# Performance work log

Hardware: AMD Instinct MI355X
Metric: run time of the kernel (lower is better)

## Reference

```python
import jax, jax.numpy as jnp
import numpy as np

B, S, E, D, H, L = 128, 50, 512, 1024, 16, 4
V, NU, NF, NR = 100000, 50000, 10000, 5
DK = D // H
FF = 4 * D


def _pe(S, D):
    # FranchisePositionalEncoding: two interleaved sin/cos halves (chrono + release*1.5)
    half = D // 2
    pos = jnp.arange(S, dtype=jnp.float32)[:, None]
    div = jnp.exp(jnp.arange(0, half, 2, dtype=jnp.float32) * (-np.log(10000.0) / half))
    def il(a):
        return jnp.stack([jnp.sin(a), jnp.cos(a)], axis=-1).reshape(S, half)
    return jnp.concatenate([il(pos * div), il(pos * div * 1.5)], axis=-1)  # [S, D]


def _ln(x, g, b):
    m = x.mean(-1, keepdims=True)
    v = ((x - m) ** 2).mean(-1, keepdims=True)
    return (x - m) * jax.lax.rsqrt(v + 1e-5) * g + b


def _gelu(x):
    return jax.nn.gelu(x, approximate=False)


def setup_inputs() -> dict:
    key = jax.random.key(0)
    ks = iter(jax.random.split(key, 64))
    def p(shape, s=0.02):
        return jax.random.normal(next(ks), shape, jnp.float32) * s
    inp = {
        'movie_table': p((V, E)), 'fran_table': p((NF, E)), 'entry_table': p((NR, E)),
        'proj_w': p((3 * E, D)), 'proj_b': jnp.zeros((D,), jnp.float32),
        'wq': p((L, D, D)), 'bq': jnp.zeros((L, D), jnp.float32),
        'wk': p((L, D, D)), 'bk': jnp.zeros((L, D), jnp.float32),
        'wv': p((L, D, D)), 'bv': jnp.zeros((L, D), jnp.float32),
        'wo': p((L, D, D)), 'bo': jnp.zeros((L, D), jnp.float32),
        'rel_table': p((L, NR, DK)),
        'aln_g': jnp.ones((L, D), jnp.float32), 'aln_b': jnp.zeros((L, D), jnp.float32),
        'f_w1': p((L, D, FF)), 'f_b1': jnp.zeros((L, FF), jnp.float32),
        'f_w2': p((L, FF, D)), 'f_b2': jnp.zeros((L, D), jnp.float32),
        'ln_g': jnp.ones((L, D), jnp.float32), 'ln_b': jnp.zeros((L, D), jnp.float32),
        'user_table': p((NU, D)),
        'mq_w': p((D, D)), 'mq_b': jnp.zeros((D,), jnp.float32),
        'mk_w': p((D, D)), 'mk_b': jnp.zeros((D,), jnp.float32),
        'mv_w': p((D, D)), 'mv_b': jnp.zeros((D,), jnp.float32),
        'mo_w': p((D, D)), 'mo_b': jnp.zeros((D,), jnp.float32),
        'c_w1': p((2 * D, D)), 'c_b1': jnp.zeros((D,), jnp.float32),
        'c_w2': p((D, 1)), 'c_b2': jnp.zeros((1,), jnp.float32),
        'n_w1': p((2 * D, D)), 'n_b1': jnp.zeros((D,), jnp.float32),
        'n_w2': p((D, V)), 'n_b2': jnp.zeros((V,), jnp.float32),
        'r_w1': p((3 * D, D)), 'r_b1': jnp.zeros((D,), jnp.float32),
        'r_w2': p((D, 1)), 'r_b2': jnp.zeros((1,), jnp.float32),
        'o_w1': p((D, D // 2)), 'o_b1': jnp.zeros((D // 2,), jnp.float32),
        'o_w2': p((D // 2, 2)), 'o_b2': jnp.zeros((2,), jnp.float32),
        'user_ids': jax.random.randint(next(ks), (B,), 0, NU),
        'movie_ids': jax.random.randint(next(ks), (B, S), 0, V),
        'franchise_ids': jax.random.randint(next(ks), (B, S), 0, NF),
        'entry_types': jax.random.randint(next(ks), (B, S), 0, NR),
        'relation_matrix': jax.random.randint(next(ks), (S, S), 0, NR),
    }
    return inp


def reference(movie_table, fran_table, entry_table, proj_w, proj_b,
              wq, bq, wk, bk, wv, bv, wo, bo, rel_table, aln_g, aln_b,
              f_w1, f_b1, f_w2, f_b2, ln_g, ln_b, user_table,
              mq_w, mq_b, mk_w, mk_b, mv_w, mv_b, mo_w, mo_b,
              c_w1, c_b1, c_w2, c_b2, n_w1, n_b1, n_w2, n_b2,
              r_w1, r_b1, r_w2, r_b2, o_w1, o_b1, o_w2, o_b2,
              user_ids, movie_ids, franchise_ids, entry_types, relation_matrix):
    b, s = movie_ids.shape
    d = proj_w.shape[1]
    nl, _, dk = rel_table.shape
    h = d // dk
    scale = 1.0 / np.sqrt(dk).astype(np.float32)

    # encoder input: concat(movie, franchise, entry) embeddings -> proj -> +PE
    x = jnp.concatenate([movie_table[movie_ids], fran_table[franchise_ids],
                         entry_table[entry_types]], axis=-1) @ proj_w + proj_b
    x = x + _pe(s, d)

    for l in range(nl):
        res = x
        q = (x @ wq[l] + bq[l]).reshape(b, s, h, dk).transpose(0, 2, 1, 3)  # [b,h,s,dk]
        k = (x @ wk[l] + bk[l]).reshape(b, s, h, dk).transpose(0, 2, 1, 3)
        v = (x @ wv[l] + bv[l]).reshape(b, s, h, dk).transpose(0, 2, 1, 3)
        scores = jnp.einsum('bhid,bhjd->bhij', q, k) * scale
        rel = rel_table[l][relation_matrix]  # [s,s,dk]
        scores = scores + 0.5 * jnp.einsum('bhid,ijd->bhij', q, rel)
        attn = jax.nn.softmax(scores, axis=-1)
        ctx = jnp.einsum('bhij,bhjd->bhid', attn, v).transpose(0, 2, 1, 3).reshape(b, s, d)
        x = _ln(ctx @ wo[l] + bo[l] + res, aln_g[l], aln_b[l])
        ff = _gelu(x @ f_w1[l] + f_b1[l]) @ f_w2[l] + f_b2[l]
        x = _ln(x + ff, ln_g[l], ln_b[l])

    # user preference cross-attention (nn.MultiheadAttention, q_len=1)
    user_emb = user_table[user_ids]  # [b,d]
    qh = (user_emb @ mq_w + mq_b).reshape(b, h, dk)
    kh = (x @ mk_w + mk_b).reshape(b, s, h, dk)
    vh = (x @ mv_w + mv_b).reshape(b, s, h, dk)
    a = jax.nn.softmax(jnp.einsum('bhd,bshd->bhs', qh, kh) * scale, axis=-1)
    user_pref = jnp.einsum('bhs,bshd->bhd', a, vh).reshape(b, d) @ mo_w + mo_b

    seq_repr = x.mean(axis=1)  # mask is None path
    ci = jnp.concatenate([user_pref, seq_repr], axis=-1)
    completion = jax.nn.sigmoid(_gelu(ci @ c_w1 + c_b1) @ c_w2 + c_b2)
    next_logits = _gelu(ci @ n_w1 + n_b1) @ n_w2 + n_b2
    ri = jnp.concatenate([user_emb, user_pref, seq_repr], axis=-1)
    rating = _gelu(ri @ r_w1 + r_b1) @ r_w2 + r_b2
    order = jax.nn.softmax(_gelu(user_pref @ o_w1 + o_b1) @ o_w2 + o_b2, axis=-1)
    return (x, completion, next_logits, rating, order, user_pref)
```

## Files before the change

### kernel.cpp

```cpp
#include <hip/hip_runtime.h>
#include <hip/hip_bf16.h>
#include <math.h>

#define B_   128
#define S_   50
#define BS_  (B_*S_)
#define E_   512
#define D_   1024
#define H_   16
#define DK_  64
#define L_   4
#define FF_  4096
#define V_   100000

typedef short bf8_t __attribute__((ext_vector_type(8)));
typedef float f32x4 __attribute__((ext_vector_type(4)));
typedef unsigned short u16;

__device__ __forceinline__ float gelu_exact(float x) {
    return 0.5f * x * (1.0f + erff(x * 0.70710678118654752440f));
}
__device__ __forceinline__ u16 f2bf(float f) {
    unsigned int u = __float_as_uint(f);
    return (u16)((u + 0x7FFFu + ((u >> 16) & 1u)) >> 16);
}
__device__ __forceinline__ float bf2f(u16 u) {
    return __uint_as_float(((unsigned int)u) << 16);
}

__device__ __forceinline__ void gload16(const u16* g, u16* l) {
    auto* g1 = reinterpret_cast<const __attribute__((address_space(1))) unsigned int*>(
                   reinterpret_cast<uintptr_t>(g));
    auto* l3 = reinterpret_cast<__attribute__((address_space(3))) unsigned int*>(
                   reinterpret_cast<uintptr_t>(l));
    __builtin_amdgcn_global_load_lds(g1, l3, 16, 0, 0);
}

__device__ __forceinline__ void wtrans_body(
    const float* __restrict__ W, u16* __restrict__ Wt,
    int K, int N, int nb, int kb, int dstRowOff)
{
    __shared__ float t[32][33];
    int c = threadIdx.x & 31, r0 = threadIdx.x >> 5;
    #pragma unroll
    for (int rr = 0; rr < 32; rr += 8)
        t[rr + r0][c] = W[(size_t)(kb + rr + r0) * N + nb + c];
    __syncthreads();
    #pragma unroll
    for (int rr = 0; rr < 32; rr += 8)
        Wt[(size_t)(dstRowOff + nb + rr + r0) * K + kb + c] = f2bf(t[c][rr + r0]);
}

__global__ __launch_bounds__(256) void wtrans(
    const float* __restrict__ W, u16* __restrict__ Wt,
    int K, int N, long srcLS, long dstLS, int dstRowOff)
{
    int l = blockIdx.z;
    wtrans_body(W + (size_t)l * srcLS, Wt + (size_t)l * dstLS,
                K, N, blockIdx.x * 32, blockIdx.y * 32, dstRowOff);
}

__global__ __launch_bounds__(256) void wtrans_qkv(
    const float* __restrict__ wq, const float* __restrict__ wk, const float* __restrict__ wv,
    u16* __restrict__ dst)
{
    int z = blockIdx.z;
    int l = z & 3, which = z >> 2;
    const float* W = (which == 0 ? wq : which == 1 ? wk : wv) + (size_t)l * (D_ * D_);
    u16* Wt = dst + (size_t)l * (3 * D_ * D_) + (size_t)which * (D_ * D_);
    wtrans_body(W, Wt, D_, D_, blockIdx.x * 32, blockIdx.y * 32, 0);
}

struct WT8 { const float* s[8]; u16* d[8]; };
__global__ __launch_bounds__(256) void wtrans8(WT8 p)
{
    int z = blockIdx.z;
    wtrans_body(p.s[z], p.d[z], D_, D_, blockIdx.x * 32, blockIdx.y * 32, 0);
}

__global__ __launch_bounds__(256) void wtrans_ff(
    const float* __restrict__ w1, const float* __restrict__ w2,
    u16* __restrict__ d1, u16* __restrict__ d2)
{
    if (blockIdx.z == 0)
        wtrans_body(w1, d1, D_, FF_, blockIdx.x * 32, blockIdx.y * 32, 0);
    else
        wtrans_body(w2, d2, FF_, D_, blockIdx.y * 32, blockIdx.x * 32, 0);
}

__global__ __launch_bounds__(256) void embed_concat(
    const float* __restrict__ mt, const float* __restrict__ ft, const float* __restrict__ et,
    const int* __restrict__ mids, const int* __restrict__ fids, const int* __restrict__ eids,
    u16* __restrict__ xinb)
{
    int bs = blockIdx.x;
    int mid = mids[bs], fid = fids[bs], eid = eids[bs];
    const float* srcs[3] = { mt + (size_t)mid * E_, ft + (size_t)fid * E_, et + (size_t)eid * E_ };
    u16* dst = xinb + (size_t)bs * (3 * E_);
    for (int i = threadIdx.x; i < 384; i += 256) {
        int seg = i >> 7, off = i & 127;
        float4 v = reinterpret_cast<const float4*>(srcs[seg])[off];
        ushort4 b;
        b.x = f2bf(v.x); b.y = f2bf(v.y); b.z = f2bf(v.z); b.w = f2bf(v.w);
        reinterpret_cast<ushort4*>(dst + seg * E_)[off] = b;
    }
}

__global__ __launch_bounds__(256) void setup_misc(
    const float* __restrict__ bq, const float* __restrict__ bk, const float* __restrict__ bv,
    const float* __restrict__ cb1, const float* __restrict__ nb1,
    const float* __restrict__ mkb, const float* __restrict__ mvb,
    float* __restrict__ bqkv, float* __restrict__ bcn, float* __restrict__ bkv,
    float* __restrict__ pet)
{
    int bi = blockIdx.x, tid = threadIdx.x;
    if (bi < 4) {
        for (int c = tid; c < 3072; c += 256) {
            float v = (c < 1024) ? bq[bi * 1024 + c]
                    : (c < 2048) ? bk[bi * 1024 + c - 1024]
                                 : bv[bi * 1024 + c - 2048];
            bqkv[bi * 3072 + c] = v;
        }
    } else if (bi == 4) {
        for (int c = tid; c < 2048; c += 256)
            bcn[c] = (c < 1024) ? cb1[c] : nb1[c - 1024];
    } else if (bi == 5) {
        for (int c = tid; c < 2048; c += 256)
            bkv[c] = (c < 1024) ? mkb[c] : mvb[c - 1024];
    } else {
        int s = bi - 6;
        const float cc = -logf(10000.0f) / 512.0f;
        for (int d = tid; d < D_; d += 256) {
            int second = d >= 512;
            int c2 = second ? d - 512 : d;
            int i = c2 >> 1;
            float div = expf(cc * (float)(2 * i));
            float aa = (float)s * div * (second ? 1.5f : 1.0f);
            pet[s * D_ + d] = (c2 & 1) ? cosf(aa) : sinf(aa);
        }
    }
}

__global__ __launch_bounds__(512, 2) void gemm256(
    const u16* __restrict__ A, int lda, const u16* __restrict__ Wt,
    const float* __restrict__ bias,
    u16* __restrict__ Cb, int ldcb,
    int N, int K, int act, const float* __restrict__ pe)
{
    __shared__ u16 As[2 * 16384];
    __shared__ u16 Bs[2 * 16384];
    const int tid  = threadIdx.x;
    const int lane = tid & 63;
    const int wid  = tid >> 6;
    const int wr   = wid >> 2;
    const int wc   = wid & 3;

    const int gx  = gridDim.x;
    const int nwg = gx * gridDim.y;
    int orig = blockIdx.y * gx + blockIdx.x;
    int qq = nwg >> 3, rr2 = nwg & 7, xcd = orig & 7, idx = orig >> 3;
    int wgid = (xcd < rr2) ? (xcd * (qq + 1) + idx)
                           : (rr2 * (qq + 1) + (xcd - rr2) * qq + idx);
    const int rowBase = (wgid / gx) * 256;
    const int colBase = (wgid % gx) * 256;

    const int fr = lane & 15;
    const int hi = lane >> 4;

    const int sRow  = lane >> 3;
    const int sChk  = (lane & 7) ^ sRow;
    const u16* aB = A  + (size_t)(rowBase + wid * 32 + sRow) * lda + sChk * 8;
    const u16* bB = Wt + (size_t)(colBase + wid * 32 + sRow) * K   + sChk * 8;
    const size_t aRowStep = (size_t)8 * lda;
    const size_t bRowStep = (size_t)8 * K;

    const int pa0 = hi ^ (fr & 7);
    const int aRd0 = (wr * 128 + fr) * 64 + pa0 * 8;
    const int aRd1 = (wr * 128 + fr) * 64 + (pa0 ^ 4) * 8;
    const int pb0 = hi ^ (fr & 7);
    const int bRd0 = (wc * 64 + fr) * 64 + pb0 * 8;
    const int bRd1 = (wc * 64 + fr) * 64 + (pb0 ^ 4) * 8;

    f32x4 acc[8][4] = {};
    const int nk = K >> 6;

    u16* Acur = As;          u16* Bcur = Bs;
    u16* Anxt = As + 16384;  u16* Bnxt = Bs + 16384;

    auto STAGE = [&](int kb, u16* dA, u16* dB) {
        #pragma unroll
        for (int i = 0; i < 4; ++i)
            gload16(aB + kb + i * aRowStep, dA + (wid * 32 + i * 8) * 64);
        #pragma unroll
        for (int i = 0; i < 4; ++i)
            gload16(bB + kb + i * bRowStep, dB + (wid * 32 + i * 8) * 64);
    };

    STAGE(0, Acur, Bcur);
    __builtin_amdgcn_sched_barrier(0);
    asm volatile("s_waitcnt vmcnt(0)\n\ts_barrier" ::: "memory");
    __builtin_amdgcn_sched_barrier(0);

    for (int t = 0; t < nk; ++t) {
        if (t + 1 < nk) {
            STAGE((t + 1) << 6, Anxt, Bnxt);
            __builtin_amdgcn_sched_barrier(0);
        }
        bf8_t bf0[4], bf1[4];
        #pragma unroll
        for (int n = 0; n < 4; ++n) {
            bf0[n] = *reinterpret_cast<const bf8_t*>(&Bcur[bRd0 + n * 1024]);
            bf1[n] = *reinterpret_cast<const bf8_t*>(&Bcur[bRd1 + n * 1024]);
        }
        __builtin_amdgcn_s_setprio(1);
        #pragma unroll
        for (int m = 0; m < 8; ++m) {
            bf8_t a0 = *reinterpret_cast<const bf8_t*>(&Acur[aRd0 + m * 1024]);
            bf8_t a1 = *reinterpret_cast<const bf8_t*>(&Acur[aRd1 + m * 1024]);
            #pragma unroll
            for (int n = 0; n < 4; ++n) {
                acc[m][n] = __builtin_amdgcn_mfma_f32_16x16x32_bf16(a0, bf0[n], acc[m][n], 0, 0, 0);
                acc[m][n] = __builtin_amdgcn_mfma_f32_16x16x32_bf16(a1, bf1[n], acc[m][n], 0, 0, 0);
            }
        }
        __builtin_amdgcn_s_setprio(0);
        if (t == nk - 1) break;
        __builtin_amdgcn_sched_barrier(0);
        asm volatile("s_waitcnt vmcnt(0) lgkmcnt(0)\n\ts_barrier" ::: "memory");
        __builtin_amdgcn_sched_barrier(0);
        u16* tp;
        tp = Acur; Acur = Anxt; Anxt = tp;
        tp = Bcur; Bcur = Bnxt; Bnxt = tp;
    }

    #pragma unroll
    for (int m = 0; m < 8; ++m) {
        int r0 = rowBase + wr * 128 + m * 16 + hi * 4;
        #pragma unroll
        for (int n = 0; n < 4; ++n) {
            int c = colBase + wc * 64 + n * 16 + fr;
            float bv = bias ? bias[c] : 0.0f;
            #pragma unroll
            for (int r = 0; r < 4; ++r) {
                float v = acc[m][n][r] + bv;
                if (act == 1) v = gelu_exact(v);
                if (pe) v += pe[(size_t)((r0 + r) % S_) * 1024 + c];
                Cb[(size_t)(r0 + r) * ldcb + c] = f2bf(v);
            }
        }
    }
}

template<int BM>
__global__ __launch_bounds__(256) void gemm_bf16_t(
    const u16* __restrict__ A, int lda, const u16* __restrict__ Wt,
    const float* __restrict__ bias, float* __restrict__ Cf,
    u16* __restrict__ Cb, int ldcb, u16* __restrict__ Cb2, int ldcb2,
    int N, int K, int act)
{
    constexpr int MR   = BM / 32;
    constexpr int AL   = BM / 64;
    constexpr int ABUF = BM * 32;
    __shared__ u16 As[2 * ABUF];
    __shared__ u16 Bs[2 * 4096];
    const int tid  = threadIdx.x;
    const int lane = tid & 63;
    const int wid  = tid >> 6;
    const int wr   = wid >> 1, wc = wid & 1;

    const int rowBase = blockIdx.y * BM;
    const int colBase = blockIdx.x * 128;

    const int fr = lane & 15;
    const int hi = lane >> 4;

    const int sRowL  = lane >> 2;
    const int sChunk = lane & 3;
    const int aRow0 = wid * (BM / 4) + sRowL;
    const int aKey  = (aRow0 >> 1) & 3;
    const u16* aS0 = A + (size_t)(rowBase + aRow0) * lda + ((sChunk ^ aKey) << 3);
    const u16* aS1 = aS0 + (size_t)16 * lda;
    const int ldsA0 = (wid * (BM / 4)) * 32;
    const int ldsA1 = ldsA0 + 512;
    const int bRow0 = wid * 32 + sRowL;
    const int bKey  = (bRow0 >> 1) & 3;
    const u16* bS0 = Wt + (size_t)(colBase + bRow0) * K + ((sChunk ^ bKey) << 3);
    const u16* bS1 = bS0 + (size_t)16 * K;
    const int ldsB0 = (wid * 32) * 32;
    const int ldsB1 = ldsB0 + 512;

    const int swz = ((hi ^ ((fr >> 1) & 3)) << 3);
    const int aRd = (wr * (BM / 2) + fr) * 32 + swz;
    const int bRd = (wc * 64 + fr) * 32 + swz;

    f32x4 acc[MR][4] = {};
    const int nk = K >> 5;

    auto STAGE = [&](int kb, int buf) {
        u16* dA = As + buf * ABUF;
        u16* dB = Bs + buf * 4096;
        gload16(aS0 + kb, dA + ldsA0);
        if constexpr (AL == 2) gload16(aS1 + kb, dA + ldsA1);
        gload16(bS0 + kb, dB + ldsB0);
        gload16(bS1 + kb, dB + ldsB1);
    };

    STAGE(0, 0);
    __builtin_amdgcn_sched_barrier(0);
    STAGE(32, 1);
    __builtin_amdgcn_sched_barrier(0);
    if constexpr (BM == 128) asm volatile("s_waitcnt vmcnt(4)\n\ts_barrier" ::: "memory");
    else                     asm volatile("s_waitcnt vmcnt(3)\n\ts_barrier" ::: "memory");
    __builtin_amdgcn_sched_barrier(0);

    for (int t = 0; t < nk; ++t) {
        const int cur = t & 1;
        const u16* bA = As + cur * ABUF;
        const u16* bB = Bs + cur * 4096;
        bf8_t af[MR], bf[4];
        #pragma unroll
        for (int m = 0; m < MR; ++m)
            af[m] = *reinterpret_cast<const bf8_t*>(&bA[aRd + m * 512]);
        #pragma unroll
        for (int n = 0; n < 4; ++n)
            bf[n] = *reinterpret_cast<const bf8_t*>(&bB[bRd + n * 512]);
        #pragma unroll
        for (int m = 0; m < MR; ++m)
            #pragma unroll
            for (int n = 0; n < 4; ++n)
                acc[m][n] = __builtin_amdgcn_mfma_f32_16x16x32_bf16(af[m], bf[n], acc[m][n], 0, 0, 0);
        if (t == nk - 1) break;
        __builtin_amdgcn_sched_barrier(0);
        asm volatile("s_waitcnt lgkmcnt(0)\n\ts_barrier" ::: "memory");
        __builtin_amdgcn_sched_barrier(0);
        if (t + 2 < nk) {
            STAGE((t + 2) << 5, cur);
            __builtin_amdgcn_sched_barrier(0);
            if constexpr (BM == 128) asm volatile("s_waitcnt vmcnt(4)\n\ts_barrier" ::: "memory");
            else                     asm volatile("s_waitcnt vmcnt(3)\n\ts_barrier" ::: "memory");
        } else {
            asm volatile("s_waitcnt vmcnt(0)\n\ts_barrier" ::: "memory");
        }
        __builtin_amdgcn_sched_barrier(0);
    }

    const int orow = hi << 2;
    #pragma unroll
    for (int m = 0; m < MR; ++m) {
        int r0 = rowBase + wr * (BM / 2) + m * 16 + orow;
        #pragma unroll
        for (int n = 0; n < 4; ++n) {
            int c = colBase + wc * 64 + n * 16 + fr;
            float bv = bias ? bias[c] : 0.0f;
            #pragma unroll
            for (int r = 0; r < 4; ++r) {
                float v = acc[m][n][r] + bv;
                if (act == 1) v = gelu_exact(v);
                if (Cf)  Cf [(size_t)(r0 + r) * N + c] = v;
                if (Cb)  Cb [(size_t)(r0 + r) * ldcb  + c] = f2bf(v);
                if (Cb2) Cb2[(size_t)(r0 + r) * ldcb2 + c] = f2bf(v);
            }
        }
    }
}

__global__ __launch_bounds__(256) void gemm_logits(
    const float* __restrict__ A, int lda, const float* __restrict__ W,
    const float* __restrict__ bias, float* __restrict__ C, int N, int K)
{
    __shared__ u16 As[2][128][40];
    __shared__ u16 Bs[2][128][40];
    const int tid  = threadIdx.x;
    const int lane = tid & 63;
    const int wid  = tid >> 6;
    const int wr   = wid >> 1, wc = wid & 1;
    const int colBase = blockIdx.x * 128;

    const int a_r = tid >> 1;
    const int a_h = (tid & 1) << 4;
    const int b_c = tid & 127;
    const int b_h = (tid >> 7) << 4;

    const int fr = lane & 15;
    const int fk = (lane >> 4) << 3;

    f32x4 acc[4][4] = {};
    const int nvalid = N - colBase;
    const bool valid = b_c < nvalid;
    const int nk = K >> 5;

    float4 aR[4];
    float  bR[16];

    auto LD = [&](int kb) {
        const float* Ap = A + (size_t)a_r * lda + kb + a_h;
        #pragma unroll
        for (int q = 0; q < 4; ++q)
            aR[q] = *reinterpret_cast<const float4*>(Ap + q * 4);
        const float* Wp = W + (size_t)(kb + b_h) * N + colBase + b_c;
        #pragma unroll
        for (int kk = 0; kk < 16; ++kk)
            bR[kk] = valid ? Wp[(size_t)kk * N] : 0.0f;
    };
    auto ST = [&](int buf) {
        #pragma unroll
        for (int q = 0; q < 4; ++q) {
            ushort4 bb;
            bb.x = f2bf(aR[q].x); bb.y = f2bf(aR[q].y);
            bb.z = f2bf(aR[q].z); bb.w = f2bf(aR[q].w);
            *reinterpret_cast<ushort4*>(&As[buf][a_r][a_h + q * 4]) = bb;
        }
        u16 tmp[16];
        #pragma unroll
        for (int kk = 0; kk < 16; ++kk) tmp[kk] = f2bf(bR[kk]);
        *reinterpret_cast<bf8_t*>(&Bs[buf][b_c][b_h])     = *reinterpret_cast<const bf8_t*>(tmp);
        *reinterpret_cast<bf8_t*>(&Bs[buf][b_c][b_h + 8]) = *reinterpret_cast<const bf8_t*>(tmp + 8);
    };

    LD(0); ST(0);
    __syncthreads();

    for (int t = 0; t < nk; ++t) {
        if (t + 1 < nk) LD((t + 1) << 5);
        const int cur = t & 1;
        bf8_t af[4], bfv[4];
        #pragma unroll
        for (int m = 0; m < 4; ++m)
            af[m] = *reinterpret_cast<const bf8_t*>(&As[cur][wr * 64 + m * 16 + fr][fk]);
        #pragma unroll
        for (int n = 0; n < 4; ++n)
            bfv[n] = *reinterpret_cast<const bf8_t*>(&Bs[cur][wc * 64 + n * 16 + fr][fk]);
        #pragma unroll
        for (int m = 0; m < 4; ++m)
            #pragma unroll
            for (int n = 0; n < 4; ++n)
                acc[m][n] = __builtin_amdgcn_mfma_f32_16x16x32_bf16(af[m], bfv[n], acc[m][n], 0, 0, 0);
        if (t + 1 < nk) ST(cur ^ 1);
        __syncthreads();
    }

    const int orow = (lane >> 4) << 2;
    #pragma unroll
    for (int m = 0; m < 4; ++m) {
        int r0 = wr * 64 + m * 16 + orow;
        #pragma unroll
        for (int n = 0; n < 4; ++n) {
            int c = colBase + wc * 64 + n * 16 + fr;
            if (c < N) {
                float bv = bias ? bias[c] : 0.0f;
                #pragma unroll
                for (int r = 0; r < 4; ++r)
                    C[(size_t)(r0 + r) * N + c] = acc[m][n][r] + bv;
            }
        }
    }
}

__global__ __launch_bounds__(256) void attn_kernel(
    const u16* __restrict__ qkv, const float* __restrict__ rt, const int* __restrict__ rm,
    u16* __restrict__ ctxb)
{
    int bh = blockIdx.x;
    int b = bh >> 4, h = bh & 15;
    __shared__ float qs[S_][DK_ + 1], ks[S_][DK_ + 1], vs[S_][DK_ + 1];
    __shared__ float rts[5][DK_];
    __shared__ float Rs[S_][8];
    int tid = threadIdx.x;
    int wave = tid >> 6, lane = tid & 63;

    for (int idx = tid; idx < S_ * DK_; idx += 256) {
        int s = idx >> 6, d = idx & 63;
        size_t g = ((size_t)(b * S_ + s)) * (3 * D_) + h * DK_ + d;
        qs[s][d] = bf2f(qkv[g]);
        ks[s][d] = bf2f(qkv[g + D_]);
        vs[s][d] = bf2f(qkv[g + 2 * D_]);
    }
    for (int i = tid; i < 5 * DK_; i += 256)
        rts[i >> 6][i & 63] = rt[i];
    __syncthreads();

    for (int t = tid; t < S_ * 5; t += 256) {
        int i = t / 5, r = t - 5 * i;
        float a = 0.0f;
        #pragma unroll 8
        for (int d = 0; d < DK_; ++d) a += qs[i][d] * rts[r][d];
        Rs[i][r] = a;
    }
    __syncthreads();

    const float scale = 0.125f;
    for (int i = wave; i < S_; i += 4) {
        float sc = -INFINITY;
        if (lane < S_) {
            float acc = 0.0f;
            #pragma unroll 8
            for (int d = 0; d < DK_; ++d) acc += qs[i][d] * ks[lane][d];
            sc = acc * scale + 0.5f * Rs[i][rm[i * S_ + lane]];
        }
        float m = sc;
        #pragma unroll
        for (int off = 32; off; off >>= 1) m = fmaxf(m, __shfl_xor(m, off));
        float e = (lane < S_) ? expf(sc - m) : 0.0f;
        float sum = e;
        #pragma unroll
        for (int off = 32; off; off >>= 1) sum += __shfl_xor(sum, off);
        float aval = e / sum;

        float acc = 0.0f;
        for (int j = 0; j < S_; ++j) {
            float aj = __shfl(aval, j);
            acc += aj * vs[j][lane];
        }
        ctxb[((size_t)(b * S_ + i)) * D_ + h * DK_ + lane] = f2bf(acc);
    }
}

__global__ __launch_bounds__(256) void add_ln(
    const u16* __restrict__ a, const u16* __restrict__ res,
    const float* __restrict__ g, const float* __restrict__ be,
    u16* __restrict__ outb, float* __restrict__ outf)
{
    int row = blockIdx.x, tid = threadIdx.x;
    int c0 = tid << 2;
    ushort4 va = *reinterpret_cast<const ushort4*>(a   + (size_t)row * D_ + c0);
    ushort4 vr = *reinterpret_cast<const ushort4*>(res + (size_t)row * D_ + c0);
    float vals[4] = { bf2f(va.x) + bf2f(vr.x), bf2f(va.y) + bf2f(vr.y),
                      bf2f(va.z) + bf2f(vr.z), bf2f(va.w) + bf2f(vr.w) };
    float s = vals[0] + vals[1] + vals[2] + vals[3];
    __shared__ float red[8];
    #pragma unroll
    for (int off = 32; off; off >>= 1) s += __shfl_xor(s, off);
    int wave = tid >> 6, lane = tid & 63;
    if (lane == 0) red[wave] = s;
    __syncthreads();
    float mean = (red[0] + red[1] + red[2] + red[3]) * (1.0f / D_);
    float vv = 0.0f;
    #pragma unroll
    for (int t = 0; t < 4; ++t) {
        float d = vals[t] - mean;
        vv += d * d;
    }
    #pragma unroll
    for (int off = 32; off; off >>= 1) vv += __shfl_xor(vv, off);
    if (lane == 0) red[4 + wave] = vv;
    __syncthreads();
    float var = (red[4] + red[5] + red[6] + red[7]) * (1.0f / D_);
    float rstd = rsqrtf(var + 1e-5f);
    float4 gv  = *reinterpret_cast<const float4*>(g  + c0);
    float4 bev = *reinterpret_cast<const float4*>(be + c0);
    float o0 = (vals[0] - mean) * rstd * gv.x + bev.x;
    float o1 = (vals[1] - mean) * rstd * gv.y + bev.y;
    float o2 = (vals[2] - mean) * rstd * gv.z + bev.z;
    float o3 = (vals[3] - mean) * rstd * gv.w + bev.w;
    ushort4 ob;
    ob.x = f2bf(o0); ob.y = f2bf(o1); ob.z = f2bf(o2); ob.w = f2bf(o3);
    *reinterpret_cast<ushort4*>(outb + (size_t)row * D_ + c0) = ob;
    if (outf) {
        float4 of = { o0, o1, o2, o3 };
        *reinterpret_cast<float4*>(outf + (size_t)row * D_ + c0) = of;
    }
}

__global__ __launch_bounds__(256) void gather_user(
    const float* __restrict__ ut, const int* __restrict__ ids,
    u16* __restrict__ o1, int ld1, u16* __restrict__ o2, int ld2)
{
    int b = blockIdx.x;
    int uid = ids[b];
    for (int d = threadIdx.x; d < D_; d += 256) {
        u16 v = f2bf(ut[(size_t)uid * D_ + d]);
        o1[(size_t)b * ld1 + d] = v;
        o2[(size_t)b * ld2 + d] = v;
    }
}

__global__ __launch_bounds__(64) void cross_attn(
    const u16* __restrict__ qh, const u16* __restrict__ kv, u16* __restrict__ up)
{
    int bh = blockIdx.x;
    int b = bh >> 4, h = bh & 15;
    int lane = threadIdx.x;
    __shared__ float qv[DK_];
    qv[lane] = bf2f(qh[(size_t)b * D_ + h * DK_ + lane]);
    __syncthreads();
    float sc = -INFINITY;
    if (lane < S_) {
        float acc = 0.0f;
        const u16* krow = kv + ((size_t)(b * S_ + lane)) * 2048 + h * DK_;
        #pragma unroll 8
        for (int d = 0; d < DK_; ++d) acc += qv[d] * bf2f(krow[d]);
        sc = acc * 0.125f;
    }
    float m = sc;
    #pragma unroll
    for (int off = 32; off; off >>= 1) m = fmaxf(m, __shfl_xor(m, off));
    float e = (lane < S_) ? expf(sc - m) : 0.0f;
    float sum = e;
    #pragma unroll
    for (int off = 32; off; off >>= 1) sum += __shfl_xor(sum, off);
    float aval = e / sum;
    float acc = 0.0f;
    for (int j = 0; j < S_; ++j) {
        float aj = __shfl(aval, j);
        acc += aj * bf2f(kv[((size_t)(b * S_ + j)) * 2048 + 1024 + h * DK_ + lane]);
    }
    up[(size_t)b * D_ + h * DK_ + lane] = f2bf(acc);
}

__global__ __launch_bounds__(256) void seq_mean(
    const float* __restrict__ x,
    u16* __restrict__ o1, int ld1, u16* __restrict__ o2, int ld2)
{
    int b = blockIdx.x;
    for (int d = threadIdx.x; d < D_; d += 256) {
        float s = 0.0f;
        for (int si = 0; si < S_; ++si)
            s += x[((size_t)(b * S_ + si)) * D_ + d];
        u16 v = f2bf(s * (1.0f / S_));
        o1[(size_t)b * ld1 + d] = v;
        o2[(size_t)b * ld2 + d] = v;
    }
}

__global__ __launch_bounds__(256) void heads_final(
    const float* __restrict__ h1cn, const float* __restrict__ h1r, const float* __restrict__ ho,
    const float* __restrict__ c_w2, const float* __restrict__ c_b2,
    const float* __restrict__ r_w2, const float* __restrict__ r_b2,
    const float* __restrict__ o_w2, const float* __restrict__ o_b2,
    float* __restrict__ comp, float* __restrict__ rating, float* __restrict__ order)
{
    int b = blockIdx.x;
    int lane = threadIdx.x & 63, wv = threadIdx.x >> 6;
    if (wv == 0) {
        float s = 0.0f;
        for (int d = lane; d < D_; d += 64) s += h1cn[(size_t)b * 2048 + d] * c_w2[d];
        #pragma unroll
        for (int off = 32; off; off >>= 1) s += __shfl_xor(s, off);
        if (lane == 0) comp[b] = 1.0f / (1.0f + expf(-(s + c_b2[0])));
    } else if (wv == 1) {
        float s = 0.0f;
        for (int d = lane; d < D_; d += 64) s += h1r[(size_t)b * D_ + d] * r_w2[d];
        #pragma unroll
        for (int off = 32; off; off >>= 1) s += __shfl_xor(s, off);
        if (lane == 0) rating[b] = s + r_b2[0];
    } else if (wv == 2) {
        float s0 = 0.0f, s1 = 0.0f;
        for (int d = lane; d < 512; d += 64) {
            float hv = ho[(size_t)b * 512 + d];
            s0 += hv * o_w2[d * 2];
            s1 += hv * o_w2[d * 2 + 1];
        }
        #pragma unroll
        for (int off = 32; off; off >>= 1) { s0 += __shfl_xor(s0, off); s1 += __shfl_xor(s1, off); }
        if (lane == 0) {
            float a = s0 + o_b2[0], c = s1 + o_b2[1];
            float m = fmaxf(a, c);
            float ea = expf(a - m), ec = expf(c - m);
            float s = ea + ec;
            order[b * 2] = ea / s;
            order[b * 2 + 1] = ec / s;
        }
    }
}

extern "C" void kernel_launch(void* const* d_in, const int* in_sizes, int n_in,
                              void* d_out, int out_size, void* d_ws, size_t ws_size,
                              hipStream_t stream) {
    const float* movie_table = (const float*)d_in[0];
    const float* fran_table  = (const float*)d_in[1];
    const float* entry_table = (const float*)d_in[2];
    const float* proj_w      = (const float*)d_in[3];
    const float* proj_b      = (const float*)d_in[4];
    const float* wq          = (const float*)d_in[5];
    const float* bq          = (const float*)d_in[6];
    const float* wk          = (const float*)d_in[7];
    const float* bk          = (const float*)d_in[8];
    const float* wv          = (const float*)d_in[9];
    const float* bv          = (const float*)d_in[10];
    const float* wo          = (const float*)d_in[11];
    const float* bo          = (const float*)d_in[12];
    const float* rel_table   = (const float*)d_in[13];
    const float* aln_g       = (const float*)d_in[14];
    const float* aln_b       = (const float*)d_in[15];
    const float* f_w1        = (const float*)d_in[16];
    const float* f_b1        = (const float*)d_in[17];
    const float* f_w2        = (const float*)d_in[18];
    const float* f_b2        = (const float*)d_in[19];
    const float* ln_g        = (const float*)d_in[20];
    const float* ln_b        = (const float*)d_in[21];
    const float* user_table  = (const float*)d_in[22];
    const float* mq_w        = (const float*)d_in[23];
    const float* mq_b        = (const float*)d_in[24];
    const float* mk_w        = (const float*)d_in[25];
    const float* mk_b        = (const float*)d_in[26];
    const float* mv_w        = (const float*)d_in[27];
    const float* mv_b        = (const float*)d_in[28];
    const float* mo_w        = (const float*)d_in[29];
    const float* mo_b        = (const float*)d_in[30];
    const float* c_w1        = (const float*)d_in[31];
    const float* c_b1        = (const float*)d_in[32];
    const float* c_w2        = (const float*)d_in[33];
    const float* c_b2        = (const float*)d_in[34];
    const float* n_w1        = (const float*)d_in[35];
    const float* n_b1        = (const float*)d_in[36];
    const float* n_w2        = (const float*)d_in[37];
    const float* n_b2        = (const float*)d_in[38];
    const float* r_w1        = (const float*)d_in[39];
    const float* r_b1        = (const float*)d_in[40];
    const float* r_w2        = (const float*)d_in[41];
    const float* r_b2        = (const float*)d_in[42];
    const float* o_w1        = (const float*)d_in[43];
    const float* o_b1        = (const float*)d_in[44];
    const float* o_w2        = (const float*)d_in[45];
    const float* o_b2        = (const float*)d_in[46];
    const int* user_ids      = (const int*)d_in[47];
    const int* movie_ids     = (const int*)d_in[48];
    const int* franchise_ids = (const int*)d_in[49];
    const int* entry_types   = (const int*)d_in[50];
    const int* relation_mat  = (const int*)d_in[51];

    u16* up16 = (u16*)d_ws;
    u16* proj_wt = up16;
    u16* wqkv_t  = proj_wt + (size_t)1024 * 1536;
    u16* wo_t    = wqkv_t  + (size_t)4 * 3072 * 1024;
    u16* fw1_buf = wo_t    + (size_t)4 * 1024 * 1024;
    u16* fw2_buf = fw1_buf + (size_t)4096 * 1024;
    u16* mq_t    = fw2_buf + (size_t)1024 * 4096;
    u16* mk_t    = mq_t    + (size_t)1024 * 1024;
    u16* mv_t    = mk_t    + (size_t)1024 * 1024;
    u16* mo_t    = mv_t    + (size_t)1024 * 1024;
    u16* cn_w1t  = mo_t    + (size_t)1024 * 1024;
    u16* r_w1t   = cn_w1t  + (size_t)2048 * 2048;
    u16* o_w1t   = r_w1t   + (size_t)1024 * 3072;
    u16* ffb     = o_w1t   + (size_t)512 * 1024;
    u16* xinb    = ffb;
    u16* xb      = ffb     + (size_t)BS_ * FF_;
    u16* xb2     = xb      + (size_t)BS_ * D_;
    u16* qkvb    = xb2     + (size_t)BS_ * D_;
    u16* kvb     = qkvb    + (size_t)BS_ * 3 * D_;
    u16* ctxb    = kvb;
    u16* ob      = kvb     + (size_t)BS_ * D_;
    u16* ueb     = kvb     + (size_t)BS_ * 2 * D_;
    u16* upb_pre = ueb     + (size_t)B_ * D_;
    u16* cib     = upb_pre + (size_t)B_ * D_;
    u16* rib     = cib     + (size_t)B_ * 2 * D_;
    float* fp    = (float*)(rib + (size_t)B_ * 3 * D_);
    float* bqkv  = fp;
    float* bcn   = bqkv + 4 * 3072;
    float* bkv   = bcn  + 2048;
    float* pet   = bkv  + 2048;
    float* h1cn  = pet  + 50 * 1024;
    float* h1r   = h1cn + (size_t)B_ * 2048;
    float* ho    = h1r  + (size_t)B_ * D_;

    float* xout    = (float*)d_out;
    float* comp    = xout + (size_t)BS_ * D_;
    float* logits  = comp + B_;
    float* rating  = logits + (size_t)B_ * V_;
    float* order   = rating + B_;
    float* upref   = order + 2 * B_;

    dim3 blk(256);
    dim3 blk512(512);

    wtrans<<<dim3(32, 48, 1), blk, 0, stream>>>(proj_w, proj_wt, 1536, 1024, 0, 0, 0);
    wtrans_qkv<<<dim3(32, 32, 12), blk, 0, stream>>>(wq, wk, wv, wqkv_t);
    WT8 w8;
    w8.s[0] = wo;                 w8.d[0] = wo_t;
    w8.s[1] = wo + 1048576;       w8.d[1] = wo_t + 1048576;
    w8.s[2] = wo + 2097152;       w8.d[2] = wo_t + 2097152;
    w8.s[3] = wo + 3145728;       w8.d[3] = wo_t + 3145728;
    w8.s[4] = mq_w;               w8.d[4] = mq_t;
    w8.s[5] = mk_w;               w8.d[5] = mk_t;
    w8.s[6] = mv_w;               w8.d[6] = mv_t;
    w8.s[7] = mo_w;               w8.d[7] = mo_t;
    wtrans8<<<dim3(32, 32, 8), blk, 0, stream>>>(w8);
    wtrans<<<dim3(32, 64, 1), blk, 0, stream>>>(c_w1, cn_w1t, 2048, 1024, 0, 0, 0);
    wtrans<<<dim3(32, 64, 1), blk, 0, stream>>>(n_w1, cn_w1t, 2048, 1024, 0, 0, 1024);
    wtrans<<<dim3(32, 96, 1), blk, 0, stream>>>(r_w1, r_w1t, 3072, 1024, 0, 0, 0);
    wtrans<<<dim3(16, 32, 1), blk, 0, stream>>>(o_w1, o_w1t, 1024, 512, 0, 0, 0);
    setup_misc<<<dim3(56), blk, 0, stream>>>(bq, bk, bv, c_b1, n_b1, mk_b, mv_b,
                                             bqkv, bcn, bkv, pet);

    embed_concat<<<BS_, blk, 0, stream>>>(movie_table, fran_table, entry_table,
                                          movie_ids, franchise_ids, entry_types, xinb);
    gemm256<<<dim3(4, 25), blk512, 0, stream>>>(xinb, 1536, proj_wt, proj_b,
                                                xb, 1024, D_, 1536, 0, pet);

    for (int l = 0; l < L_; ++l) {
        gemm256<<<dim3(12, 25), blk512, 0, stream>>>(xb, 1024,
                wqkv_t + (size_t)l * 3145728, bqkv + l * 3072,
                qkvb, 3072, 3 * D_, D_, 0, nullptr);
        attn_kernel<<<B_ * H_, blk, 0, stream>>>(qkvb, rel_table + (size_t)l * 5 * DK_,
                                                 relation_mat, ctxb);
        gemm256<<<dim3(4, 25), blk512, 0, stream>>>(ctxb, 1024,
                wo_t + (size_t)l * 1048576, bo + l * D_,
                ob, 1024, D_, D_, 0, nullptr);
        add_ln<<<BS_, blk, 0, stream>>>(ob, xb, aln_g + l * D_, aln_b + l * D_, xb2, nullptr);
        wtrans_ff<<<dim3(128, 32, 2), blk, 0, stream>>>(f_w1 + (size_t)l * D_ * FF_,
                                                        f_w2 + (size_t)l * FF_ * D_,
                                                        fw1_buf, fw2_buf);
        gemm256<<<dim3(16, 25), blk512, 0, stream>>>(xb2, 1024, fw1_buf, f_b1 + l * FF_,
                ffb, 4096, FF_, D_, 1, nullptr);
        gemm256<<<dim3(4, 25), blk512, 0, stream>>>(ffb, 4096, fw2_buf, f_b2 + l * D_,
                ob, 1024, D_, FF_, 0, nullptr);
        add_ln<<<BS_, blk, 0, stream>>>(ob, xb2, ln_g + l * D_, ln_b + l * D_, xb,
                                        (l == L_ - 1) ? xout : nullptr);
    }

    gather_user<<<B_, blk, 0, stream>>>(user_table, user_ids, ueb, 1024, rib, 3072);
    gemm_bf16_t<64><<<dim3(8, 2), blk, 0, stream>>>(ueb, 1024, mq_t, mq_b,
            nullptr, qkvb, 1024, nullptr, 0, D_, D_, 0);
    gemm256<<<dim3(8, 25), blk512, 0, stream>>>(xb, 1024, mk_t, bkv,
            kvb, 2048, 2 * D_, D_, 0, nullptr);
    cross_attn<<<B_ * H_, dim3(64), 0, stream>>>(qkvb, kvb, upb_pre);
    gemm_bf16_t<64><<<dim3(8, 2), blk, 0, stream>>>(upb_pre, 1024, mo_t, mo_b,
            upref, cib, 2048, rib + 1024, 3072, D_, D_, 0);

    seq_mean<<<B_, blk, 0, stream>>>(xout, cib + 1024, 2048, rib + 2048, 3072);

    gemm_bf16_t<64><<<dim3(16, 2), blk, 0, stream>>>(cib, 2048, cn_w1t, bcn,
            h1cn, nullptr, 0, nullptr, 0, 2048, 2048, 1);
    gemm_bf16_t<64><<<dim3(8, 2), blk, 0, stream>>>(rib, 3072, r_w1t, r_b1,
            h1r, nullptr, 0, nullptr, 0, D_, 3072, 1);
    gemm_bf16_t<64><<<dim3(4, 2), blk, 0, stream>>>(cib, 2048, o_w1t, o_b1,
            ho, nullptr, 0, nullptr, 0, 512, D_, 1);
    gemm_logits<<<dim3(782, 1), blk, 0, stream>>>(h1cn + 1024, 2048, n_w2, n_b2,
                                                  logits, V_, D_);
    heads_final<<<B_, blk, 0, stream>>>(h1cn, h1r, ho, c_w2, c_b2, r_w2, r_b2,
                                        o_w2, o_b2, comp, rating, order);
}
```

Baseline: 2.345 ms.

## Split GEMM K-tile into half-tiles with interleaved loads and partial waits

Restructures the 256x256 bf16 MFMA GEMM main loop. Shared-memory tiles are now laid out as two 32-wide K halves with a new XOR swizzle. Global loads for the next tile are issued in four chunks between MFMA phases, and the loop waits with vmcnt(4) instead of draining all loads, so copy and compute overlap more finely. Launch bounds drop to one workgroup per CU to free registers. The risks are lower occupancy, more barriers per K step, and new swizzle indexing that must match the read pattern exactly.

Result: no change. 2.359 ms (+0.6%).

```diff
diff --git a/kernel.cpp b/kernel.cpp
--- a/kernel.cpp
+++ b/kernel.cpp
@@ -141,7 +141,7 @@
     }
 }
 
-__global__ __launch_bounds__(512, 2) void gemm256(
+__global__ __launch_bounds__(512, 1) void gemm256(
     const u16* __restrict__ A, int lda, const u16* __restrict__ Wt,
     const float* __restrict__ bias,
     u16* __restrict__ Cb, int ldcb,
@@ -167,19 +167,20 @@
     const int fr = lane & 15;
     const int hi = lane >> 4;
 
-    const int sRow  = lane >> 3;
-    const int sChk  = (lane & 7) ^ sRow;
-    const u16* aB = A  + (size_t)(rowBase + wid * 32 + sRow) * lda + sChk * 8;
-    const u16* bB = Wt + (size_t)(colBase + wid * 32 + sRow) * K   + sChk * 8;
-    const size_t aRowStep = (size_t)8 * lda;
-    const size_t bRowStep = (size_t)8 * K;
-
-    const int pa0 = hi ^ (fr & 7);
-    const int aRd0 = (wr * 128 + fr) * 64 + pa0 * 8;
-    const int aRd1 = (wr * 128 + fr) * 64 + (pa0 ^ 4) * 8;
-    const int pb0 = hi ^ (fr & 7);
-    const int bRd0 = (wc * 64 + fr) * 64 + pb0 * 8;
-    const int bRd1 = (wc * 64 + fr) * 64 + (pb0 ^ 4) * 8;
+    const int slot0 = wid * 64 + lane;
+    const int slot1 = slot0 + 512;
+    const int r0s = slot0 >> 2, p0s = slot0 & 3;
+    const int r1s = slot1 >> 2, p1s = slot1 & 3;
+    const u16* aSrc0 = A  + (size_t)(rowBase + r0s) * lda + ((p0s ^ ((r0s >> 1) & 3)) << 3);
+    const u16* aSrc1 = A  + (size_t)(rowBase + r1s) * lda + ((p1s ^ ((r1s >> 1) & 3)) << 3);
+    const u16* bSrc0 = Wt + (size_t)(colBase + r0s) * K   + ((p0s ^ ((r0s >> 1) & 3)) << 3);
+    const u16* bSrc1 = Wt + (size_t)(colBase + r1s) * K   + ((p1s ^ ((r1s >> 1) & 3)) << 3);
+    const int dOff0 = slot0 * 8;
+    const int dOff1 = slot1 * 8;
+
+    const int key  = (fr >> 1) & 3;
+    const int aRdC = (wr * 128 + fr) * 32 + ((hi ^ key) << 3);
+    const int bRdC = (wc * 64  + fr) * 32 + ((hi ^ key) << 3);
 
     f32x4 acc[8][4] = {};
     const int nk = K >> 6;
@@ -187,47 +188,89 @@
     u16* Acur = As;          u16* Bcur = Bs;
     u16* Anxt = As + 16384;  u16* Bnxt = Bs + 16384;
 
-    auto STAGE = [&](int kb, u16* dA, u16* dB) {
-        #pragma unroll
-        for (int i = 0; i < 4; ++i)
-            gload16(aB + kb + i * aRowStep, dA + (wid * 32 + i * 8) * 64);
-        #pragma unroll
-        for (int i = 0; i < 4; ++i)
-            gload16(bB + kb + i * bRowStep, dB + (wid * 32 + i * 8) * 64);
-    };
-
-    STAGE(0, Acur, Bcur);
+    gload16(aSrc0, Acur + dOff0);          gload16(aSrc1, Acur + dOff1);
     __builtin_amdgcn_sched_barrier(0);
-    asm volatile("s_waitcnt vmcnt(0)\n\ts_barrier" ::: "memory");
+    gload16(bSrc0, Bcur + dOff0);          gload16(bSrc1, Bcur + dOff1);
     __builtin_amdgcn_sched_barrier(0);
+    gload16(aSrc0 + 32, Acur + 8192 + dOff0); gload16(aSrc1 + 32, Acur + 8192 + dOff1);
+    __builtin_amdgcn_sched_barrier(0);
+    gload16(bSrc0 + 32, Bcur + 8192 + dOff0); gload16(bSrc1 + 32, Bcur + 8192 + dOff1);
+    __builtin_amdgcn_sched_barrier(0);
 
     for (int t = 0; t < nk; ++t) {
-        if (t + 1 < nk) {
-            STAGE((t + 1) << 6, Anxt, Bnxt);
-            __builtin_amdgcn_sched_barrier(0);
-        }
-        bf8_t bf0[4], bf1[4];
-        #pragma unroll
-        for (int n = 0; n < 4; ++n) {
-            bf0[n] = *reinterpret_cast<const bf8_t*>(&Bcur[bRd0 + n * 1024]);
-            bf1[n] = *reinterpret_cast<const bf8_t*>(&Bcur[bRd1 + n * 1024]);
-        }
+        const bool st = (t + 1 < nk);
+        const int kb1 = (t + 1) << 6;
+        bf8_t bfr[4], afr[4];
+
+        asm volatile("s_waitcnt vmcnt(4)" ::: "memory");
+        __builtin_amdgcn_s_barrier();
+        __builtin_amdgcn_sched_barrier(0);
+        #pragma unroll
+        for (int n = 0; n < 4; ++n)
+            bfr[n] = *reinterpret_cast<const bf8_t*>(&Bcur[n * 512 + bRdC]);
+        #pragma unroll
+        for (int m = 0; m < 4; ++m)
+            afr[m] = *reinterpret_cast<const bf8_t*>(&Acur[m * 512 + aRdC]);
+        if (st) { gload16(aSrc0 + kb1, Anxt + dOff0); gload16(aSrc1 + kb1, Anxt + dOff1); }
+        __builtin_amdgcn_sched_barrier(0);
         __builtin_amdgcn_s_setprio(1);
         #pragma unroll
-        for (int m = 0; m < 8; ++m) {
-            bf8_t a0 = *reinterpret_cast<const bf8_t*>(&Acur[aRd0 + m * 1024]);
-            bf8_t a1 = *reinterpret_cast<const bf8_t*>(&Acur[aRd1 + m * 1024]);
+        for (int m = 0; m < 4; ++m)
             #pragma unroll
-            for (int n = 0; n < 4; ++n) {
-                acc[m][n] = __builtin_amdgcn_mfma_f32_16x16x32_bf16(a0, bf0[n], acc[m][n], 0, 0, 0);
-                acc[m][n] = __builtin_amdgcn_mfma_f32_16x16x32_bf16(a1, bf1[n], acc[m][n], 0, 0, 0);
-            }
-        }
+            for (int n = 0; n < 4; ++n)
+                acc[m][n] = __builtin_amdgcn_mfma_f32_16x16x32_bf16(afr[m], bfr[n], acc[m][n], 0, 0, 0);
         __builtin_amdgcn_s_setprio(0);
-        if (t == nk - 1) break;
-        __builtin_amdgcn_sched_barrier(0);
-        asm volatile("s_waitcnt vmcnt(0) lgkmcnt(0)\n\ts_barrier" ::: "memory");
-        __builtin_amdgcn_sched_barrier(0);
+        __builtin_amdgcn_s_barrier();
+        __builtin_amdgcn_sched_barrier(0);
+
+        #pragma unroll
+        for (int m = 0; m < 4; ++m)
+            afr[m] = *reinterpret_cast<const bf8_t*>(&Acur[2048 + m * 512 + aRdC]);
+        if (st) { gload16(bSrc0 + kb1, Bnxt + dOff0); gload16(bSrc1 + kb1, Bnxt + dOff1); }
+        __builtin_amdgcn_sched_barrier(0);
+        __builtin_amdgcn_s_setprio(1);
+        #pragma unroll
+        for (int m = 0; m < 4; ++m)
+            #pragma unroll
+            for (int n = 0; n < 4; ++n)
+                acc[4 + m][n] = __builtin_amdgcn_mfma_f32_16x16x32_bf16(afr[m], bfr[n], acc[4 + m][n], 0, 0, 0);
+        __builtin_amdgcn_s_setprio(0);
+
+        if (st) asm volatile("s_waitcnt vmcnt(4)" ::: "memory");
+        else    asm volatile("s_waitcnt vmcnt(0)" ::: "memory");
+        __builtin_amdgcn_s_barrier();
+        __builtin_amdgcn_sched_barrier(0);
+        #pragma unroll
+        for (int n = 0; n < 4; ++n)
+            bfr[n] = *reinterpret_cast<const bf8_t*>(&Bcur[8192 + n * 512 + bRdC]);
+        #pragma unroll
+        for (int m = 0; m < 4; ++m)
+            afr[m] = *reinterpret_cast<const bf8_t*>(&Acur[8192 + m * 512 + aRdC]);
+        if (st) { gload16(aSrc0 + kb1 + 32, Anxt + 8192 + dOff0); gload16(aSrc1 + kb1 + 32, Anxt + 8192 + dOff1); }
+        __builtin_amdgcn_sched_barrier(0);
+        __builtin_amdgcn_s_setprio(1);
+        #pragma unroll
+        for (int m = 0; m < 4; ++m)
+            #pragma unroll
+            for (int n = 0; n < 4; ++n)
+                acc[m][n] = __builtin_amdgcn_mfma_f32_16x16x32_bf16(afr[m], bfr[n], acc[m][n], 0, 0, 0);
+        __builtin_amdgcn_s_setprio(0);
+        __builtin_amdgcn_s_barrier();
+        __builtin_amdgcn_sched_barrier(0);
+
+        #pragma unroll
+        for (int m = 0; m < 4; ++m)
+            afr[m] = *reinterpret_cast<const bf8_t*>(&Acur[8192 + 2048 + m * 512 + aRdC]);
+        if (st) { gload16(bSrc0 + kb1 + 32, Bnxt + 8192 + dOff0); gload16(bSrc1 + kb1 + 32, Bnxt + 8192 + dOff1); }
+        __builtin_amdgcn_sched_barrier(0);
+        __builtin_amdgcn_s_setprio(1);
+        #pragma unroll
+        for (int m = 0; m < 4; ++m)
+            #pragma unroll
+            for (int n = 0; n < 4; ++n)
+                acc[4 + m][n] = __builtin_amdgcn_mfma_f32_16x16x32_bf16(afr[m], bfr[n], acc[4 + m][n], 0, 0, 0);
+        __builtin_amdgcn_s_setprio(0);
+
         u16* tp;
         tp = Acur; Acur = Anxt; Anxt = tp;
         tp = Bcur; Bcur = Bnxt; Bnxt = tp;
```
